# Performance work log

Hardware: AMD Instinct MI355X
Metric: run time of the kernel (lower is better)

Reference implementation:

```python
import jax, jax.numpy as jnp
import numpy as np

EMBED = 512
HEADS = 8
FMUL = 4
TAU = 2.0
V_TH = 1.0      # spiking threshold (spikingjelly default)
ALPHA = 2.0     # ATan surrogate alpha (spikingjelly default)
EPS = 1e-5


@jax.custom_vjp
def spike_fn(v):
    # Heaviside spike with ATan surrogate gradient (spikingjelly surrogate.ATan)
    return (v >= V_TH).astype(v.dtype)

def _spike_fwd(v):
    return spike_fn(v), v

def _spike_bwd(v, g):
    t = (jnp.pi / 2.0) * ALPHA * (v - V_TH)
    return (g * (ALPHA / 2.0) / (1.0 + t * t),)

spike_fn.defvjp(_spike_fwd, _spike_bwd)


def layernorm(x, g, b):
    mu = jnp.mean(x, axis=-1, keepdims=True)
    var = jnp.mean(jnp.square(x - mu), axis=-1, keepdims=True)
    return (x - mu) * jax.lax.rsqrt(var + EPS) * g + b


def setup_inputs() -> dict:
    key = jax.random.key(0)
    ks = jax.random.split(key, 12)
    m, s, e = 4, 2048, EMBED
    f = e * FMUL
    sc = 0.02
    return {
        "x":  jax.random.normal(ks[0], (m, s, e), jnp.float32),
        "wq": jax.random.normal(ks[1], (e, e), jnp.float32) * sc,
        "bq": jnp.zeros((e,), jnp.float32),
        "wk": jax.random.normal(ks[2], (e, e), jnp.float32) * sc,
        "bk": jnp.zeros((e,), jnp.float32),
        "wv": jax.random.normal(ks[3], (e, e), jnp.float32) * sc,
        "bv": jnp.zeros((e,), jnp.float32),
        "w1": jax.random.normal(ks[4], (e, f), jnp.float32) * sc,
        "b1": jnp.zeros((f,), jnp.float32),
        "w2": jax.random.normal(ks[5], (f, e), jnp.float32) * sc,
        "b2": jnp.zeros((e,), jnp.float32),
        "g1": jnp.ones((e,), jnp.float32),
        "be1": jnp.zeros((e,), jnp.float32),
        "g2": jnp.ones((e,), jnp.float32),
        "be2": jnp.zeros((e,), jnp.float32),
    }


def reference(x, wq, bq, wk, bk, wv, bv, w1, b1, w2, b2, g1, be1, g2, be2):
    m, s, e = x.shape
    h = HEADS
    d = e // h

    # --- pre-norm attention (NOTE: original has NO 1/sqrt(d) scaling) ---
    n1 = layernorm(x, g1, be1)
    q = (n1 @ wq + bq).reshape(m, s, h, d).transpose(0, 2, 1, 3)  # [m,h,s,d]
    k = (n1 @ wk + bk).reshape(m, s, h, d).transpose(0, 2, 1, 3)
    v = (n1 @ wv + bv).reshape(m, s, h, d).transpose(0, 2, 1, 3)
    scores = jnp.einsum('bhqd,bhkd->bhqk', q, k)       # [m,h,s,s], unscaled
    attn = jax.nn.softmax(scores, axis=-1)
    ctx = jnp.einsum('bhqk,bhkd->bhqd', attn, v)       # [m,h,s,d]
    att_out = ctx.transpose(0, 2, 1, 3).reshape(m, s, e)

    x = x + att_out
    # dropout p=0.4 is identity at inference (eval path in the original)

    # --- FFN with spiking activation ---
    n2 = layernorm(x, g2, be2)
    h1 = n2 @ w1 + b1                                  # [m,s,4e]
    # single-step LIF charge from v=0: v = v + (x - v)/tau = x/tau
    spikes = spike_fn(h1 / TAU)
    return x + (spikes @ w2 + b2)
```

## Files before the change

kernel.cpp:

```cpp
#include <hip/hip_runtime.h>
#include <stdint.h>

#define EMB 512
#define SEQ 2048
#define MB 4
#define NH 8
#define HD 64
#define ROWS (MB*SEQ)
#define MARGIN 0.02f
#define CAP 65536
#define LOG2E 1.44269504f
#define EXPB (-17.3123405f)

typedef unsigned short u16;
typedef __attribute__((ext_vector_type(8))) short bf16x8;
typedef __attribute__((ext_vector_type(4))) float f32x4;
typedef __attribute__((ext_vector_type(2))) unsigned int u32x2;
typedef __attribute__((ext_vector_type(4))) unsigned int u32x4;

union Frag { u32x2 u[2]; bf16x8 v; };
union Frag4 { unsigned u[4]; bf16x8 v; };

__device__ __forceinline__ u16 f2bf(float f) {
  union { float f; unsigned u; } a; a.f = f;
  unsigned r = a.u + 0x7FFFu + ((a.u >> 16) & 1u);
  return (u16)(r >> 16);
}
__device__ __forceinline__ void gld16(const void* g, void* l) {
  __builtin_amdgcn_global_load_lds(
      (const __attribute__((address_space(1))) void*)g,
      (__attribute__((address_space(3))) void*)l, 16, 0, 0);
}


__global__ void k_transpose_all(const float* __restrict__ wq, const float* __restrict__ wk,
                                const float* __restrict__ wv, const float* __restrict__ w1,
                                u16* __restrict__ wqkvT, u16* __restrict__ w1T) {
  __shared__ float tile[32][33];
  int b = blockIdx.x;
  const float* src; u16* dst; int N, bx, by;
  if (b < 768) {
    int z = b >> 8, rem = b & 255; bx = rem & 15; by = rem >> 4; N = 512;
    src = (z == 0) ? wq : ((z == 1) ? wk : wv);
    dst = wqkvT + z * 512 * 512;
  } else {
    int rem = b - 768; bx = rem & 63; by = rem >> 6; N = 2048;
    src = w1; dst = w1T;
  }
  int tx = threadIdx.x, ty = threadIdx.y;
  int k0 = by * 32, n0 = bx * 32;
  for (int i = 0; i < 32; i += 8)
    tile[ty + i][tx] = src[(size_t)(k0 + ty + i) * N + n0 + tx];
  __syncthreads();
  for (int i = 0; i < 32; i += 8)
    dst[(size_t)(n0 + ty + i) * 512 + k0 + tx] = f2bf(tile[tx][ty + i]);
}

__global__ __launch_bounds__(256) void k_ln1(const float* __restrict__ x,
    const float* __restrict__ g, const float* __restrict__ b, u16* __restrict__ n1,
    int* __restrict__ cnt) {
  if (blockIdx.x == 0 && threadIdx.x < 2) cnt[threadIdx.x] = 0;
  int wid = threadIdx.x >> 6, lane = threadIdx.x & 63;
  int row = blockIdx.x * 4 + wid;
  const float* xr = x + (size_t)row * EMB + lane * 8;
  f32x4 v0 = *(const f32x4*)xr;
  f32x4 v1 = *(const f32x4*)(xr + 4);
  float s = v0.x+v0.y+v0.z+v0.w + v1.x+v1.y+v1.z+v1.w;
  float q = v0.x*v0.x+v0.y*v0.y+v0.z*v0.z+v0.w*v0.w
          + v1.x*v1.x+v1.y*v1.y+v1.z*v1.z+v1.w*v1.w;
  #pragma unroll
  for (int o = 1; o < 64; o <<= 1) { s += __shfl_xor(s, o); q += __shfl_xor(q, o); }
  float mu = s * (1.0f/512.0f);
  float rs = 1.0f / sqrtf(q * (1.0f/512.0f) - mu*mu + 1e-5f);
  f32x4 ga = *(const f32x4*)(g + lane*8), gb = *(const f32x4*)(g + lane*8 + 4);
  f32x4 ba = *(const f32x4*)(b + lane*8), bb = *(const f32x4*)(b + lane*8 + 4);
  union { u16 h[8]; u32x4 v; } o8;
  o8.h[0] = f2bf((v0.x-mu)*rs*ga.x + ba.x); o8.h[1] = f2bf((v0.y-mu)*rs*ga.y + ba.y);
  o8.h[2] = f2bf((v0.z-mu)*rs*ga.z + ba.z); o8.h[3] = f2bf((v0.w-mu)*rs*ga.w + ba.w);
  o8.h[4] = f2bf((v1.x-mu)*rs*gb.x + bb.x); o8.h[5] = f2bf((v1.y-mu)*rs*gb.y + bb.y);
  o8.h[6] = f2bf((v1.z-mu)*rs*gb.z + bb.z); o8.h[7] = f2bf((v1.w-mu)*rs*gb.w + bb.w);
  *(u32x4*)(n1 + (size_t)row * EMB + lane * 8) = o8.v;
}

__global__ __launch_bounds__(256) void k_ln2(const float* __restrict__ x,
    const float* __restrict__ att, const float* __restrict__ g, const float* __restrict__ b,
    const float* __restrict__ b2, float* __restrict__ x2, u16* __restrict__ n2,
    float* __restrict__ out) {
  int wid = threadIdx.x >> 6, lane = threadIdx.x & 63;
  int row = blockIdx.x * 4 + wid;
  size_t base = (size_t)row * EMB + lane * 8;
  f32x4 v0 = *(const f32x4*)(x + base)     + *(const f32x4*)(att + base);
  f32x4 v1 = *(const f32x4*)(x + base + 4) + *(const f32x4*)(att + base + 4);
  *(f32x4*)(x2 + base) = v0;
  *(f32x4*)(x2 + base + 4) = v1;
  *(f32x4*)(out + base)     = v0 + *(const f32x4*)(b2 + lane*8);
  *(f32x4*)(out + base + 4) = v1 + *(const f32x4*)(b2 + lane*8 + 4);
  float s = v0.x+v0.y+v0.z+v0.w + v1.x+v1.y+v1.z+v1.w;
  float q = v0.x*v0.x+v0.y*v0.y+v0.z*v0.z+v0.w*v0.w
          + v1.x*v1.x+v1.y*v1.y+v1.z*v1.z+v1.w*v1.w;
  #pragma unroll
  for (int o = 1; o < 64; o <<= 1) { s += __shfl_xor(s, o); q += __shfl_xor(q, o); }
  float mu = s * (1.0f/512.0f);
  float rs = 1.0f / sqrtf(q * (1.0f/512.0f) - mu*mu + 1e-5f);
  f32x4 ga = *(const f32x4*)(g + lane*8), gb = *(const f32x4*)(g + lane*8 + 4);
  f32x4 ba = *(const f32x4*)(b + lane*8), bb = *(const f32x4*)(b + lane*8 + 4);
  union { u16 h[8]; u32x4 v; } o8;
  o8.h[0] = f2bf((v0.x-mu)*rs*ga.x + ba.x); o8.h[1] = f2bf((v0.y-mu)*rs*ga.y + ba.y);
  o8.h[2] = f2bf((v0.z-mu)*rs*ga.z + ba.z); o8.h[3] = f2bf((v0.w-mu)*rs*ga.w + ba.w);
  o8.h[4] = f2bf((v1.x-mu)*rs*gb.x + bb.x); o8.h[5] = f2bf((v1.y-mu)*rs*gb.y + bb.y);
  o8.h[6] = f2bf((v1.z-mu)*rs*gb.z + bb.z); o8.h[7] = f2bf((v1.w-mu)*rs*gb.w + bb.w);
  *(u32x4*)(n2 + (size_t)row * EMB + lane * 8) = o8.v;
}

#define GEMM_CORE(A_, Bt_, m0_, n0_)                                           \
  __shared__ u16 As[2][128 * 32];                                              \
  __shared__ u16 Bs[2][128 * 32];                                              \
  int tid = threadIdx.x;                                                       \
  int wid = tid >> 6, lane = tid & 63;                                         \
  int quad = lane >> 4, ln15 = lane & 15;                                      \
  int wm = (wid >> 1) * 64, wn = (wid & 1) * 64;                               \
  int arow = lane >> 2, acol = (lane & 3) * 8;                                 \
  const u16* gA0 = A_  + (size_t)(m0_ + wid * 32 + arow) * 512 + acol;         \
  const u16* gA1 = gA0 + (size_t)16 * 512;                                     \
  const u16* gB0 = Bt_ + (size_t)(n0_ + wid * 32 + arow) * 512 + acol;         \
  const u16* gB1 = gB0 + (size_t)16 * 512;                                     \
  f32x4 acc[4][4] = {};                                                        \
  gld16(gA0, &As[0][(wid * 32) * 32]); gld16(gA1, &As[0][(wid * 32 + 16) * 32]);\
  gld16(gB0, &Bs[0][(wid * 32) * 32]); gld16(gB1, &Bs[0][(wid * 32 + 16) * 32]);\
  for (int kt = 0; kt < 16; kt++) {                                            \
    int cur = kt & 1;                                                          \
    __syncthreads();                                                           \
    if (kt < 15) {                                                             \
      int ko = (kt + 1) * 32;                                                  \
      gld16(gA0 + ko, &As[cur ^ 1][(wid * 32) * 32]);                          \
      gld16(gA1 + ko, &As[cur ^ 1][(wid * 32 + 16) * 32]);                     \
      gld16(gB0 + ko, &Bs[cur ^ 1][(wid * 32) * 32]);                          \
      gld16(gB1 + ko, &Bs[cur ^ 1][(wid * 32 + 16) * 32]);                     \
    }                                                                          \
    bf16x8 af[4], bf[4];                                                       \
    _Pragma("unroll")                                                          \
    for (int i = 0; i < 4; i++) {                                              \
      af[i] = *(const bf16x8*)&As[cur][(wm + i * 16 + ln15) * 32 + quad * 8];  \
      bf[i] = *(const bf16x8*)&Bs[cur][(wn + i * 16 + ln15) * 32 + quad * 8];  \
    }                                                                          \
    _Pragma("unroll")                                                          \
    for (int i = 0; i < 4; i++)                                                \
      _Pragma("unroll")                                                        \
      for (int j = 0; j < 4; j++)                                              \
        acc[i][j] = __builtin_amdgcn_mfma_f32_16x16x32_bf16(af[i], bf[j],      \
                                                            acc[i][j], 0, 0, 0);\
  }                                                                            \
  __syncthreads();

__global__ __launch_bounds__(256) void k_gemm_qkv(
    const u16* __restrict__ A, const u16* __restrict__ Bt,
    const float* __restrict__ bq, const float* __restrict__ bk, const float* __restrict__ bv,
    u16* __restrict__ Qb, u16* __restrict__ Kb, u16* __restrict__ Vtb) {
  int m0 = blockIdx.y * 128, n0 = blockIdx.x * 128;
  GEMM_CORE(A, Bt, m0, n0)
  #pragma unroll
  for (int j = 0; j < 4; j++) {
    int n = n0 + wn + j * 16 + ln15;
    int t = n >> 9, cc = n & 511, head = cc >> 6, dd = cc & 63;
    float bias = (t == 0) ? bq[cc] : ((t == 1) ? bk[cc] : bv[cc]);
    #pragma unroll
    for (int i = 0; i < 4; i++) {
      int row0 = m0 + wm + i * 16 + quad * 4;
      int mm = row0 >> 11, ss0 = row0 & 2047;
      if (t == 2) {
        union { u16 h[4]; u32x2 v; } pk;
        #pragma unroll
        for (int r = 0; r < 4; r++) pk.h[r] = f2bf(acc[i][j][r] + bias);
        *(u32x2*)(Vtb + ((size_t)(mm * 8 + head) * 64 + dd) * 2048 + ss0) = pk.v;
      } else {
        u16* dst = (t == 0) ? Qb : Kb;
        #pragma unroll
        for (int r = 0; r < 4; r++)
          dst[((size_t)(mm * 8 + head) * 2048 + ss0 + r) * 64 + dd] =
              f2bf(acc[i][j][r] + bias);
      }
    }
  }
}

__global__ __launch_bounds__(256) void k_gemm_ffn1(
    const u16* __restrict__ A, const u16* __restrict__ Bt, const float* __restrict__ b1,
    int* __restrict__ cnt, unsigned* __restrict__ spikeL, unsigned* __restrict__ candL) {
  int m0 = blockIdx.y * 128, n0 = blockIdx.x * 128;
  GEMM_CORE(A, Bt, m0, n0)
  #pragma unroll
  for (int j = 0; j < 4; j++) {
    int n = n0 + wn + j * 16 + ln15;
    float bias = b1[n];
    #pragma unroll
    for (int i = 0; i < 4; i++) {
      #pragma unroll
      for (int r = 0; r < 4; r++) {
        int row = m0 + wm + i * 16 + quad * 4 + r;
        float hv = acc[i][j][r] + bias;
        if (hv >= 2.0f - MARGIN) {
          if (hv >= 2.0f + MARGIN) {
            int ix = atomicAdd(&cnt[0], 1);
            if (ix < CAP) spikeL[ix] = (unsigned)(row * 2048 + n);
          } else {
            int ix = atomicAdd(&cnt[1], 1);
            if (ix < CAP) candL[ix] = (unsigned)(row * 2048 + n);
          }
        }
      }
    }
  }
}

#define F_STAGE(BUF, T0)                                                       \
  do {                                                                         \
    gld16(gK0 + (size_t)(T0)       * 4096, &L.SB[BUF][0][0][rb0 * 64]);        \
    gld16(gK1 + (size_t)(T0)       * 4096, &L.SB[BUF][0][0][rb1 * 64]);        \
    gld16(gK0 + (size_t)((T0) + 1) * 4096, &L.SB[BUF][0][1][rb0 * 64]);        \
    gld16(gK1 + (size_t)((T0) + 1) * 4096, &L.SB[BUF][0][1][rb1 * 64]);        \
    gld16(gV0 + (T0) * 64,       &L.SB[BUF][1][0][rb0 * 64]);                  \
    gld16(gV1 + (T0) * 64,       &L.SB[BUF][1][0][rb1 * 64]);                  \
    gld16(gV0 + ((T0) + 1) * 64, &L.SB[BUF][1][1][rb0 * 64]);                  \
    gld16(gV1 + ((T0) + 1) * 64, &L.SB[BUF][1][1][rb1 * 64]);                  \
  } while (0)

#define F_INNER(BUF, SUB)                                                      \
  do {                                                                         \
    const u16* Kc = L.SB[BUF][0][SUB];                                         \
    const u16* Vc = L.SB[BUF][1][SUB];                                         \
    f32x4 s4[2][4];                                                            \
    _Pragma("unroll")                                                          \
    for (int j = 0; j < 4; j++) {                                              \
      bf16x8 a = *(const bf16x8*)(Kc + (j * 16 + ln15) * 64 + ((quad ^ lm) * 8)); \
      s4[0][j] = __builtin_amdgcn_mfma_f32_16x16x32_bf16(a, aQ[0][0].v, z4, 0, 0, 0); \
      s4[1][j] = __builtin_amdgcn_mfma_f32_16x16x32_bf16(a, aQ[1][0].v, z4, 0, 0, 0); \
    }                                                                          \
    _Pragma("unroll")                                                          \
    for (int j = 0; j < 4; j++) {                                              \
      bf16x8 a = *(const bf16x8*)(Kc + (j * 16 + ln15) * 64 + (((4 + quad) ^ lm) * 8)); \
      s4[0][j] = __builtin_amdgcn_mfma_f32_16x16x32_bf16(a, aQ[0][1].v, s4[0][j], 0, 0, 0); \
      s4[1][j] = __builtin_amdgcn_mfma_f32_16x16x32_bf16(a, aQ[1][1].v, s4[1][j], 0, 0, 0); \
    }                                                                          \
    Frag4 bP[2][2];                                                            \
    _Pragma("unroll")                                                          \
    for (int h = 0; h < 2; h++) {                                              \
      unsigned pr[4][4];                                                       \
      _Pragma("unroll")                                                        \
      for (int j = 0; j < 4; j++)                                              \
        _Pragma("unroll")                                                      \
        for (int r = 0; r < 4; r++) {                                          \
          float p = __builtin_amdgcn_exp2f(fmaf(s4[h][j][r], LOG2E, EXPB));    \
          l[h] += p;                                                           \
          union { float f; unsigned u; } cc; cc.f = p;                         \
          pr[j][r] = cc.u;                                                     \
        }                                                                      \
      _Pragma("unroll")                                                        \
      for (int t = 0; t < 2; t++) {                                            \
        bP[h][t].u[0] = __builtin_amdgcn_perm(pr[2*t][1],   pr[2*t][0],   0x07060302u); \
        bP[h][t].u[1] = __builtin_amdgcn_perm(pr[2*t][3],   pr[2*t][2],   0x07060302u); \
        bP[h][t].u[2] = __builtin_amdgcn_perm(pr[2*t+1][1], pr[2*t+1][0], 0x07060302u); \
        bP[h][t].u[3] = __builtin_amdgcn_perm(pr[2*t+1][3], pr[2*t+1][2], 0x07060302u); \
      }                                                                        \
    }                                                                          \
    _Pragma("unroll")                                                          \
    for (int t = 0; t < 2; t++)                                                \
      _Pragma("unroll")                                                        \
      for (int j = 0; j < 4; j++) {                                            \
        int row = j * 16 + ln15;                                               \
        int c0 = 4 * t + (quad >> 1), sub = (quad & 1) * 4;                    \
        Frag aV;                                                               \
        aV.u[0] = *(const u32x2*)(Vc + row * 64 + ((c0 ^ lm) * 8) + sub);      \
        aV.u[1] = *(const u32x2*)(Vc + row * 64 + (((c0 + 2) ^ lm) * 8) + sub);\
        U[0][j] = __builtin_amdgcn_mfma_f32_16x16x32_bf16(aV.v, bP[0][t].v,    \
                                                          U[0][j], 0, 0, 0);   \
        U[1][j] = __builtin_amdgcn_mfma_f32_16x16x32_bf16(aV.v, bP[1][t].v,    \
                                                          U[1][j], 0, 0, 0);   \
      }                                                                        \
  } while (0)

#define F_STEP(CUR, S)                                                         \
  do {                                                                         \
    __syncthreads();                                                           \
    if ((S) < 15) F_STAGE((CUR) ^ 1, 2 * (S) + 2);                             \
    F_INNER(CUR, 0);                                                           \
    F_INNER(CUR, 1);                                                           \
  } while (0)

__global__ __launch_bounds__(256, 2) void k_flash(
    const u16* __restrict__ Q, const u16* __restrict__ K,
    const u16* __restrict__ Vt, float* __restrict__ att) {
  __shared__ union {
    u16 SB[2][2][2][64 * 64];
    float T[4][16 * 68];
  } L;
  int tid = threadIdx.x, wid = tid >> 6, lane = tid & 63;
  int quad = lane >> 4, ln15 = lane & 15, lm = ln15 & 7;
  int qb = blockIdx.x, head = blockIdx.y, mm = blockIdx.z;
  int mh = mm * 8 + head;
  const u16* Qp = Q  + (size_t)mh * SEQ * HD;
  const u16* Kp = K  + (size_t)mh * SEQ * HD;
  const u16* Vp = Vt + (size_t)mh * HD * SEQ;
  int q0 = qb * 128 + wid * 32;

  Frag aQ[2][2];
  #pragma unroll
  for (int h = 0; h < 2; h++)
    #pragma unroll
    for (int t = 0; t < 2; t++) {
      u32x4 g = *(const u32x4*)(Qp + (size_t)(q0 + h * 16 + ln15) * 64 + t * 32 + quad * 8);
      aQ[h][t].u[0].x = g.x; aQ[h][t].u[0].y = g.y;
      aQ[h][t].u[1].x = g.z; aQ[h][t].u[1].y = g.w;
    }
  const f32x4 z4 = {0.f, 0.f, 0.f, 0.f};

  int srow = lane >> 3;
  int sch  = (lane & 7) ^ (srow & 7);
  int rb0 = wid * 16, rb1 = wid * 16 + 8;
  const u16* gK0 = Kp + (size_t)(rb0 + srow) * 64 + sch * 8;
  const u16* gK1 = Kp + (size_t)(rb1 + srow) * 64 + sch * 8;
  const u16* gV0 = Vp + (size_t)(rb0 + srow) * SEQ + sch * 8;
  const u16* gV1 = Vp + (size_t)(rb1 + srow) * SEQ + sch * 8;

  float l[2] = {0.f, 0.f};
  f32x4 U[2][4] = {};

  F_STAGE(0, 0);
  for (int it = 0; it < 8; it++) {
    F_STEP(0, 2 * it);
    F_STEP(1, 2 * it + 1);
  }
  __syncthreads();

  #pragma unroll
  for (int h = 0; h < 2; h++) {
    float lv = l[h];
    lv += __shfl_xor(lv, 16);
    lv += __shfl_xor(lv, 32);
    float rl = 1.0f / lv;
    float* Tw = L.T[wid];
    #pragma unroll
    for (int j = 0; j < 4; j++)
      *(f32x4*)(Tw + ln15 * 68 + j * 16 + quad * 4) = U[h][j] * rl;
    #pragma unroll
    for (int s = 0; s < 4; s++) {
      f32x4 o = *(const f32x4*)(Tw + (quad * 4 + s) * 68 + ln15 * 4);
      *(f32x4*)(att + ((size_t)mm * SEQ + q0 + h * 16 + quad * 4 + s) * EMB +
                head * 64 + ln15 * 4) = o;
    }
  }
}

__global__ __launch_bounds__(256) void k_fixup(
    const float* __restrict__ x2, const float* __restrict__ w1, const float* __restrict__ b1,
    const float* __restrict__ g2, const float* __restrict__ be2,
    int* __restrict__ cnt, unsigned* __restrict__ spikeL, const unsigned* __restrict__ candL) {
  __shared__ float sb[8];
  int tid = threadIdx.x;
  int nC = cnt[1]; if (nC > CAP) nC = CAP;
  for (int e = blockIdx.x; e < nC; e += gridDim.x) {
    unsigned v = candL[e];
    int row = (int)(v >> 11), col = (int)(v & 2047u);
    const float* xr = x2 + (size_t)row * 512;
    float x0 = xr[tid], x1 = xr[tid + 256];
    float s = x0 + x1, q = x0 * x0 + x1 * x1;
    #pragma unroll
    for (int o = 1; o < 64; o <<= 1) { s += __shfl_xor(s, o); q += __shfl_xor(q, o); }
    if ((tid & 63) == 0) { sb[tid >> 6] = s; sb[4 + (tid >> 6)] = q; }
    __syncthreads();
    float st = sb[0] + sb[1] + sb[2] + sb[3];
    float qt = sb[4] + sb[5] + sb[6] + sb[7];
    __syncthreads();
    float mu = st * (1.f / 512.f);
    float rs = 1.f / sqrtf(qt * (1.f / 512.f) - mu * mu + 1e-5f);
    float na = (x0 - mu) * rs * g2[tid] + be2[tid];
    float nb = (x1 - mu) * rs * g2[tid + 256] + be2[tid + 256];
    float dd = na * w1[(size_t)tid * 2048 + col] + nb * w1[(size_t)(tid + 256) * 2048 + col];
    #pragma unroll
    for (int o = 1; o < 64; o <<= 1) dd += __shfl_xor(dd, o);
    if ((tid & 63) == 0) sb[tid >> 6] = dd;
    __syncthreads();
    if (tid == 0) {
      float hv = sb[0] + sb[1] + sb[2] + sb[3] + b1[col];
      if (hv >= 2.0f) { int ix = atomicAdd(&cnt[0], 1); if (ix < CAP) spikeL[ix] = v; }
    }
    __syncthreads();
  }
}

__global__ void k_apply(const float* __restrict__ w2, const int* __restrict__ cnt,
                        const unsigned* __restrict__ spikeL, float* __restrict__ out) {
  int n = cnt[0]; if (n > CAP) n = CAP;
  int tid = threadIdx.x;
  for (int e = blockIdx.x; e < n; e += gridDim.x) {
    unsigned v = spikeL[e];
    int row = (int)(v >> 11), col = (int)(v & 2047u);
    atomicAdd(&out[(size_t)row * 512 + tid * 2 + 0], w2[(size_t)col * 512 + tid * 2 + 0]);
    atomicAdd(&out[(size_t)row * 512 + tid * 2 + 1], w2[(size_t)col * 512 + tid * 2 + 1]);
  }
}


extern "C" void kernel_launch(void* const* d_in, const int* in_sizes, int n_in,
                              void* d_out, int out_size, void* d_ws, size_t ws_size,
                              hipStream_t stream) {
  (void)in_sizes; (void)n_in; (void)out_size; (void)ws_size;
  const float* x   = (const float*)d_in[0];
  const float* wq  = (const float*)d_in[1];
  const float* bq  = (const float*)d_in[2];
  const float* wk  = (const float*)d_in[3];
  const float* bk  = (const float*)d_in[4];
  const float* wv  = (const float*)d_in[5];
  const float* bv  = (const float*)d_in[6];
  const float* w1  = (const float*)d_in[7];
  const float* b1  = (const float*)d_in[8];
  const float* w2  = (const float*)d_in[9];
  const float* b2  = (const float*)d_in[10];
  const float* g1  = (const float*)d_in[11];
  const float* be1 = (const float*)d_in[12];
  const float* g2  = (const float*)d_in[13];
  const float* be2 = (const float*)d_in[14];
  float* out = (float*)d_out;

  char* w = (char*)d_ws;
  size_t off = 0;
  auto take = [&](size_t bytes) { char* p = w + off; off += (bytes + 255) & ~(size_t)255; return p; };
  int*      cnt    = (int*)take(256);
  u16*      n1     = (u16*)take((size_t)ROWS * EMB * 2);
  u16*      wqkvT  = (u16*)take((size_t)1536 * 512 * 2);
  u16*      w1T    = (u16*)take((size_t)2048 * 512 * 2);
  u16*      Qb     = (u16*)take((size_t)MB * NH * SEQ * HD * 2);
  u16*      Kb     = (u16*)take((size_t)MB * NH * SEQ * HD * 2);
  u16*      Vtb    = (u16*)take((size_t)MB * NH * SEQ * HD * 2);
  float*    att    = (float*)take((size_t)ROWS * EMB * 4);
  float*    x2     = (float*)take((size_t)ROWS * EMB * 4);
  u16*      n2     = (u16*)take((size_t)ROWS * EMB * 2);
  unsigned* spikeL = (unsigned*)take((size_t)CAP * 4);
  unsigned* candL  = (unsigned*)take((size_t)CAP * 4);

  k_transpose_all<<<1792, dim3(32, 8), 0, stream>>>(wq, wk, wv, w1, wqkvT, w1T);
  k_ln1<<<ROWS / 4, 256, 0, stream>>>(x, g1, be1, n1, cnt);
  k_gemm_qkv<<<dim3(12, 64), 256, 0, stream>>>(n1, wqkvT, bq, bk, bv, Qb, Kb, Vtb);
  k_flash<<<dim3(16, 8, 4), 256, 0, stream>>>(Qb, Kb, Vtb, att);
  k_ln2<<<ROWS / 4, 256, 0, stream>>>(x, att, g2, be2, b2, x2, n2, out);
  k_gemm_ffn1<<<dim3(16, 64), 256, 0, stream>>>(n2, w1T, b1, cnt, spikeL, candL);
  k_fixup<<<256, 256, 0, stream>>>(x2, w1, b1, g2, be2, cnt, spikeL, candL);
  k_apply<<<128, 256, 0, stream>>>(w2, cnt, spikeL, out);
}
```

Measured before the change: 211.2 us.

## Fuse weight transpose with LN1, store attention in bf16, use 64-wide GEMM k-stages

Result: slower. 216.2 us (+2.4%).

```diff
diff --git a/kernel.cpp b/kernel.cpp
--- a/kernel.cpp
+++ b/kernel.cpp
@@ -26,6 +26,12 @@
   unsigned r = a.u + 0x7FFFu + ((a.u >> 16) & 1u);
   return (u16)(r >> 16);
 }
+__device__ __forceinline__ float bflo(unsigned u) {
+  union { unsigned u; float f; } c; c.u = u << 16; return c.f;
+}
+__device__ __forceinline__ float bfhi(unsigned u) {
+  union { unsigned u; float f; } c; c.u = u & 0xffff0000u; return c.f;
+}
 __device__ __forceinline__ void gld16(const void* g, void* l) {
   __builtin_amdgcn_global_load_lds(
       (const __attribute__((address_space(1))) void*)g,
@@ -33,64 +39,69 @@
 }
 
 
-__global__ void k_transpose_all(const float* __restrict__ wq, const float* __restrict__ wk,
-                                const float* __restrict__ wv, const float* __restrict__ w1,
-                                u16* __restrict__ wqkvT, u16* __restrict__ w1T) {
+__global__ __launch_bounds__(256) void k_prep(
+    const float* __restrict__ x, const float* __restrict__ g1, const float* __restrict__ be1,
+    const float* __restrict__ wq, const float* __restrict__ wk,
+    const float* __restrict__ wv, const float* __restrict__ w1,
+    u16* __restrict__ n1, u16* __restrict__ wqkvT, u16* __restrict__ w1T,
+    int* __restrict__ cnt) {
   __shared__ float tile[32][33];
-  int b = blockIdx.x;
-  const float* src; u16* dst; int N, bx, by;
-  if (b < 768) {
-    int z = b >> 8, rem = b & 255; bx = rem & 15; by = rem >> 4; N = 512;
-    src = (z == 0) ? wq : ((z == 1) ? wk : wv);
-    dst = wqkvT + z * 512 * 512;
+  int b = blockIdx.x, tid = threadIdx.x;
+  if (b < 1792) {
+    const float* src; u16* dst; int N, bx, by;
+    if (b < 768) {
+      int z = b >> 8, rem = b & 255; bx = rem & 15; by = rem >> 4; N = 512;
+      src = (z == 0) ? wq : ((z == 1) ? wk : wv);
+      dst = wqkvT + z * 512 * 512;
+    } else {
+      int rem = b - 768; bx = rem & 63; by = rem >> 6; N = 2048;
+      src = w1; dst = w1T;
+    }
+    int tx = tid & 31, ty = tid >> 5;
+    int k0 = by * 32, n0 = bx * 32;
+    for (int i = 0; i < 32; i += 8)
+      tile[ty + i][tx] = src[(size_t)(k0 + ty + i) * N + n0 + tx];
+    __syncthreads();
+    for (int i = 0; i < 32; i += 8)
+      dst[(size_t)(n0 + ty + i) * 512 + k0 + tx] = f2bf(tile[tx][ty + i]);
   } else {
-    int rem = b - 768; bx = rem & 63; by = rem >> 6; N = 2048;
-    src = w1; dst = w1T;
-  }
-  int tx = threadIdx.x, ty = threadIdx.y;
-  int k0 = by * 32, n0 = bx * 32;
-  for (int i = 0; i < 32; i += 8)
-    tile[ty + i][tx] = src[(size_t)(k0 + ty + i) * N + n0 + tx];
-  __syncthreads();
-  for (int i = 0; i < 32; i += 8)
-    dst[(size_t)(n0 + ty + i) * 512 + k0 + tx] = f2bf(tile[tx][ty + i]);
-}
-
-__global__ __launch_bounds__(256) void k_ln1(const float* __restrict__ x,
-    const float* __restrict__ g, const float* __restrict__ b, u16* __restrict__ n1,
-    int* __restrict__ cnt) {
-  if (blockIdx.x == 0 && threadIdx.x < 2) cnt[threadIdx.x] = 0;
-  int wid = threadIdx.x >> 6, lane = threadIdx.x & 63;
-  int row = blockIdx.x * 4 + wid;
-  const float* xr = x + (size_t)row * EMB + lane * 8;
-  f32x4 v0 = *(const f32x4*)xr;
-  f32x4 v1 = *(const f32x4*)(xr + 4);
-  float s = v0.x+v0.y+v0.z+v0.w + v1.x+v1.y+v1.z+v1.w;
-  float q = v0.x*v0.x+v0.y*v0.y+v0.z*v0.z+v0.w*v0.w
-          + v1.x*v1.x+v1.y*v1.y+v1.z*v1.z+v1.w*v1.w;
-  #pragma unroll
-  for (int o = 1; o < 64; o <<= 1) { s += __shfl_xor(s, o); q += __shfl_xor(q, o); }
-  float mu = s * (1.0f/512.0f);
-  float rs = 1.0f / sqrtf(q * (1.0f/512.0f) - mu*mu + 1e-5f);
-  f32x4 ga = *(const f32x4*)(g + lane*8), gb = *(const f32x4*)(g + lane*8 + 4);
-  f32x4 ba = *(const f32x4*)(b + lane*8), bb = *(const f32x4*)(b + lane*8 + 4);
-  union { u16 h[8]; u32x4 v; } o8;
-  o8.h[0] = f2bf((v0.x-mu)*rs*ga.x + ba.x); o8.h[1] = f2bf((v0.y-mu)*rs*ga.y + ba.y);
-  o8.h[2] = f2bf((v0.z-mu)*rs*ga.z + ba.z); o8.h[3] = f2bf((v0.w-mu)*rs*ga.w + ba.w);
-  o8.h[4] = f2bf((v1.x-mu)*rs*gb.x + bb.x); o8.h[5] = f2bf((v1.y-mu)*rs*gb.y + bb.y);
-  o8.h[6] = f2bf((v1.z-mu)*rs*gb.z + bb.z); o8.h[7] = f2bf((v1.w-mu)*rs*gb.w + bb.w);
-  *(u32x4*)(n1 + (size_t)row * EMB + lane * 8) = o8.v;
+    if (b == 1792 && tid < 2) cnt[tid] = 0;
+    int wid = tid >> 6, lane = tid & 63;
+    int row = (b - 1792) * 4 + wid;
+    const float* xr = x + (size_t)row * EMB + lane * 8;
+    f32x4 v0 = *(const f32x4*)xr;
+    f32x4 v1 = *(const f32x4*)(xr + 4);
+    float s = v0.x+v0.y+v0.z+v0.w + v1.x+v1.y+v1.z+v1.w;
+    float q = v0.x*v0.x+v0.y*v0.y+v0.z*v0.z+v0.w*v0.w
+            + v1.x*v1.x+v1.y*v1.y+v1.z*v1.z+v1.w*v1.w;
+    #pragma unroll
+    for (int o = 1; o < 64; o <<= 1) { s += __shfl_xor(s, o); q += __shfl_xor(q, o); }
+    float mu = s * (1.0f/512.0f);
+    float rs = 1.0f / sqrtf(q * (1.0f/512.0f) - mu*mu + 1e-5f);
+    f32x4 ga = *(const f32x4*)(g1 + lane*8), gb = *(const f32x4*)(g1 + lane*8 + 4);
+    f32x4 ba = *(const f32x4*)(be1 + lane*8), bb = *(const f32x4*)(be1 + lane*8 + 4);
+    union { u16 h[8]; u32x4 v; } o8;
+    o8.h[0] = f2bf((v0.x-mu)*rs*ga.x + ba.x); o8.h[1] = f2bf((v0.y-mu)*rs*ga.y + ba.y);
+    o8.h[2] = f2bf((v0.z-mu)*rs*ga.z + ba.z); o8.h[3] = f2bf((v0.w-mu)*rs*ga.w + ba.w);
+    o8.h[4] = f2bf((v1.x-mu)*rs*gb.x + bb.x); o8.h[5] = f2bf((v1.y-mu)*rs*gb.y + bb.y);
+    o8.h[6] = f2bf((v1.z-mu)*rs*gb.z + bb.z); o8.h[7] = f2bf((v1.w-mu)*rs*gb.w + bb.w);
+    *(u32x4*)(n1 + (size_t)row * EMB + lane * 8) = o8.v;
+  }
 }
 
 __global__ __launch_bounds__(256) void k_ln2(const float* __restrict__ x,
-    const float* __restrict__ att, const float* __restrict__ g, const float* __restrict__ b,
+    const u16* __restrict__ att, const float* __restrict__ g, const float* __restrict__ b,
     const float* __restrict__ b2, float* __restrict__ x2, u16* __restrict__ n2,
     float* __restrict__ out) {
   int wid = threadIdx.x >> 6, lane = threadIdx.x & 63;
   int row = blockIdx.x * 4 + wid;
   size_t base = (size_t)row * EMB + lane * 8;
-  f32x4 v0 = *(const f32x4*)(x + base)     + *(const f32x4*)(att + base);
-  f32x4 v1 = *(const f32x4*)(x + base + 4) + *(const f32x4*)(att + base + 4);
+  u32x4 av = *(const u32x4*)(att + base);
+  f32x4 t0, t1;
+  t0.x = bflo(av.x); t0.y = bfhi(av.x); t0.z = bflo(av.y); t0.w = bfhi(av.y);
+  t1.x = bflo(av.z); t1.y = bfhi(av.z); t1.z = bflo(av.w); t1.w = bfhi(av.w);
+  f32x4 v0 = *(const f32x4*)(x + base)     + t0;
+  f32x4 v1 = *(const f32x4*)(x + base + 4) + t1;
   *(f32x4*)(x2 + base) = v0;
   *(f32x4*)(x2 + base + 4) = v1;
   *(f32x4*)(out + base)     = v0 + *(const f32x4*)(b2 + lane*8);
@@ -112,9 +123,46 @@
   *(u32x4*)(n2 + (size_t)row * EMB + lane * 8) = o8.v;
 }
 
+#define G_STAGE(BUF, T0)                                                       \
+  do {                                                                         \
+    int ko = (T0) * 32;                                                        \
+    gld16(gA0 + ko,      &As[BUF][0][(wid * 32) * 32]);                        \
+    gld16(gA1 + ko,      &As[BUF][0][(wid * 32 + 16) * 32]);                   \
+    gld16(gA0 + ko + 32, &As[BUF][1][(wid * 32) * 32]);                        \
+    gld16(gA1 + ko + 32, &As[BUF][1][(wid * 32 + 16) * 32]);                   \
+    gld16(gB0 + ko,      &Bs[BUF][0][(wid * 32) * 32]);                        \
+    gld16(gB1 + ko,      &Bs[BUF][0][(wid * 32 + 16) * 32]);                   \
+    gld16(gB0 + ko + 32, &Bs[BUF][1][(wid * 32) * 32]);                        \
+    gld16(gB1 + ko + 32, &Bs[BUF][1][(wid * 32 + 16) * 32]);                   \
+  } while (0)
+
+#define G_INNER(CUR, SUB)                                                      \
+  do {                                                                         \
+    bf16x8 af[4], bf[4];                                                       \
+    _Pragma("unroll")                                                          \
+    for (int i = 0; i < 4; i++) {                                              \
+      af[i] = *(const bf16x8*)&As[CUR][SUB][(wm + i * 16 + ln15) * 32 + quad * 8]; \
+      bf[i] = *(const bf16x8*)&Bs[CUR][SUB][(wn + i * 16 + ln15) * 32 + quad * 8]; \
+    }                                                                          \
+    _Pragma("unroll")                                                          \
+    for (int i = 0; i < 4; i++)                                                \
+      _Pragma("unroll")                                                        \
+      for (int j = 0; j < 4; j++)                                              \
+        acc[i][j] = __builtin_amdgcn_mfma_f32_16x16x32_bf16(af[i], bf[j],      \
+                                                            acc[i][j], 0, 0, 0);\
+  } while (0)
+
+#define G_STEP(CUR, S)                                                         \
+  do {                                                                         \
+    __syncthreads();                                                           \
+    if ((S) < 7) G_STAGE((CUR) ^ 1, 2 * (S) + 2);                              \
+    G_INNER(CUR, 0);                                                           \
+    G_INNER(CUR, 1);                                                           \
+  } while (0)
+
 #define GEMM_CORE(A_, Bt_, m0_, n0_)                                           \
-  __shared__ u16 As[2][128 * 32];                                              \
-  __shared__ u16 Bs[2][128 * 32];                                              \
+  __shared__ u16 As[2][2][128 * 32];                                           \
+  __shared__ u16 Bs[2][2][128 * 32];                                           \
   int tid = threadIdx.x;                                                       \
   int wid = tid >> 6, lane = tid & 63;                                         \
   int quad = lane >> 4, ln15 = lane & 15;                                      \
@@ -125,30 +173,10 @@
   const u16* gB0 = Bt_ + (size_t)(n0_ + wid * 32 + arow) * 512 + acol;         \
   const u16* gB1 = gB0 + (size_t)16 * 512;                                     \
   f32x4 acc[4][4] = {};                                                        \
-  gld16(gA0, &As[0][(wid * 32) * 32]); gld16(gA1, &As[0][(wid * 32 + 16) * 32]);\
-  gld16(gB0, &Bs[0][(wid * 32) * 32]); gld16(gB1, &Bs[0][(wid * 32 + 16) * 32]);\
-  for (int kt = 0; kt < 16; kt++) {                                            \
-    int cur = kt & 1;                                                          \
-    __syncthreads();                                                           \
-    if (kt < 15) {                                                             \
-      int ko = (kt + 1) * 32;                                                  \
-      gld16(gA0 + ko, &As[cur ^ 1][(wid * 32) * 32]);                          \
-      gld16(gA1 + ko, &As[cur ^ 1][(wid * 32 + 16) * 32]);                     \
-      gld16(gB0 + ko, &Bs[cur ^ 1][(wid * 32) * 32]);                          \
-      gld16(gB1 + ko, &Bs[cur ^ 1][(wid * 32 + 16) * 32]);                     \
-    }                                                                          \
-    bf16x8 af[4], bf[4];                                                       \
-    _Pragma("unroll")                                                          \
-    for (int i = 0; i < 4; i++) {                                              \
-      af[i] = *(const bf16x8*)&As[cur][(wm + i * 16 + ln15) * 32 + quad * 8];  \
-      bf[i] = *(const bf16x8*)&Bs[cur][(wn + i * 16 + ln15) * 32 + quad * 8];  \
-    }                                                                          \
-    _Pragma("unroll")                                                          \
-    for (int i = 0; i < 4; i++)                                                \
-      _Pragma("unroll")                                                        \
-      for (int j = 0; j < 4; j++)                                              \
-        acc[i][j] = __builtin_amdgcn_mfma_f32_16x16x32_bf16(af[i], bf[j],      \
-                                                            acc[i][j], 0, 0, 0);\
+  G_STAGE(0, 0);                                                               \
+  for (int it = 0; it < 4; it++) {                                             \
+    G_STEP(0, 2 * it);                                                         \
+    G_STEP(1, 2 * it + 1);                                                     \
   }                                                                            \
   __syncthreads();
 
@@ -288,7 +316,7 @@
 
 __global__ __launch_bounds__(256, 2) void k_flash(
     const u16* __restrict__ Q, const u16* __restrict__ K,
-    const u16* __restrict__ Vt, float* __restrict__ att) {
+    const u16* __restrict__ Vt, u16* __restrict__ att) {
   __shared__ union {
     u16 SB[2][2][2][64 * 64];
     float T[4][16 * 68];
@@ -344,8 +372,11 @@
     #pragma unroll
     for (int s = 0; s < 4; s++) {
       f32x4 o = *(const f32x4*)(Tw + (quad * 4 + s) * 68 + ln15 * 4);
-      *(f32x4*)(att + ((size_t)mm * SEQ + q0 + h * 16 + quad * 4 + s) * EMB +
-                head * 64 + ln15 * 4) = o;
+      union { u16 h4[4]; u32x2 v; } pk;
+      pk.h4[0] = f2bf(o.x); pk.h4[1] = f2bf(o.y);
+      pk.h4[2] = f2bf(o.z); pk.h4[3] = f2bf(o.w);
+      *(u32x2*)(att + ((size_t)mm * SEQ + q0 + h * 16 + quad * 4 + s) * EMB +
+                head * 64 + ln15 * 4) = pk.v;
     }
   }
 }
@@ -431,14 +462,13 @@
   u16*      Qb     = (u16*)take((size_t)MB * NH * SEQ * HD * 2);
   u16*      Kb     = (u16*)take((size_t)MB * NH * SEQ * HD * 2);
   u16*      Vtb    = (u16*)take((size_t)MB * NH * SEQ * HD * 2);
-  float*    att    = (float*)take((size_t)ROWS * EMB * 4);
+  u16*      att    = (u16*)take((size_t)ROWS * EMB * 2);
   float*    x2     = (float*)take((size_t)ROWS * EMB * 4);
   u16*      n2     = (u16*)take((size_t)ROWS * EMB * 2);
   unsigned* spikeL = (unsigned*)take((size_t)CAP * 4);
   unsigned* candL  = (unsigned*)take((size_t)CAP * 4);
 
-  k_transpose_all<<<1792, dim3(32, 8), 0, stream>>>(wq, wk, wv, w1, wqkvT, w1T);
-  k_ln1<<<ROWS / 4, 256, 0, stream>>>(x, g1, be1, n1, cnt);
+  k_prep<<<3840, 256, 0, stream>>>(x, g1, be1, wq, wk, wv, w1, n1, wqkvT, w1T, cnt);
   k_gemm_qkv<<<dim3(12, 64), 256, 0, stream>>>(n1, wqkvT, bq, bk, bv, Qb, Kb, Vtb);
   k_flash<<<dim3(16, 8, 4), 256, 0, stream>>>(Qb, Kb, Vtb, att);
   k_ln2<<<ROWS / 4, 256, 0, stream>>>(x, att, g2, be2, b2, x2, n2, out);
```
